# Kernel optimization log

Hardware: AMD Instinct MI355X
Metric: run time of the kernel (lower is better)

## Reference

```python
import jax, jax.numpy as jnp
import numpy as np

V = 8000; TZ = 128; TU = 256; B = 64; H = 1024; E = 512; DG = 64
GI = E + 2 * H + DG  # GRU input size = embed + z_ctx + u_ctx + degree


def _build_sparse_z(rng):
    # faithful vectorized version of get_sparse_selective_input (minus vocab SLOT branch)
    z_np = rng.integers(0, V + 10, size=(TZ, B))  # some ids >= V -> OOV copy path
    res = np.full((TZ, B, V + TZ), 1e-10, np.float32)
    w = z_np[:-1]                                   # [TZ-1, B]
    cond = (w == 2) | (w >= V)
    ti, bi = np.meshgrid(np.arange(TZ - 1), np.arange(B), indexing='ij')
    col = np.where(cond, V + ti, w)
    val = np.where(cond, np.float32(5.0), np.float32(1.0))
    res[ti + 1, bi, col] = val
    return jnp.asarray(res.transpose(1, 0, 2))      # [B, TZ, V+TZ]


def setup_inputs():
    key = jax.random.key(0)
    ks = jax.random.split(key, 16)
    s = 0.02
    iv = 1.0 / np.sqrt(H)
    return dict(
        z_enc_out=jax.random.normal(ks[0], (TZ, B, H), jnp.float32),
        u_enc_out=jax.random.normal(ks[1], (TU, B, H), jnp.float32),
        m_t_input=jax.random.randint(ks[2], (1, B), 0, V),
        degree_input=jax.random.normal(ks[3], (B, DG), jnp.float32),
        last_hidden=jax.random.normal(ks[4], (1, B, H), jnp.float32),
        sparse_z_input=_build_sparse_z(np.random.default_rng(0)),
        emb_W=jax.random.normal(ks[5], (V, E), jnp.float32) * s,
        attn_z_W=jax.random.normal(ks[6], (H, 2 * H), jnp.float32) * s,
        attn_z_b=jnp.zeros((H,), jnp.float32),
        attn_z_v=jax.random.normal(ks[7], (H,), jnp.float32) * iv,
        attn_u_W=jax.random.normal(ks[8], (H, 2 * H), jnp.float32) * s,
        attn_u_b=jnp.zeros((H,), jnp.float32),
        attn_u_v=jax.random.normal(ks[9], (H,), jnp.float32) * iv,
        gru_Wih=jax.random.normal(ks[10], (3 * H, GI), jnp.float32) * s,
        gru_Whh=jax.random.normal(ks[11], (3 * H, H), jnp.float32) * s,
        gru_bih=jnp.zeros((3 * H,), jnp.float32),
        gru_bhh=jnp.zeros((3 * H,), jnp.float32),
        proj_W=jax.random.normal(ks[12], (V, 3 * H), jnp.float32) * s,
        proj_b=jnp.zeros((V,), jnp.float32),
        copy2_W=jax.random.normal(ks[13], (H, H), jnp.float32) * s,
        copy2_b=jnp.zeros((H,), jnp.float32),
    )


def _attn(hidden, enc, W, b, v):
    # hidden [1,B,H], enc [T,B,H] -> context [1,B,H] (Bahdanau additive attention)
    enc_b = jnp.transpose(enc, (1, 0, 2))                       # [B,T,H]
    Hrep = jnp.broadcast_to(jnp.transpose(hidden, (1, 0, 2)), enc_b.shape)
    energy = jnp.tanh(jnp.concatenate([Hrep, enc_b], -1) @ W.T + b)  # [B,T,H]
    scores = jnp.einsum('bth,h->bt', energy, v)[:, None, :]    # [B,1,T]
    alpha = jax.nn.softmax(scores, axis=2)
    ctx = jnp.einsum('bit,bth->bih', alpha, enc_b)              # [B,1,H]
    return jnp.transpose(ctx, (1, 0, 2))                        # [1,B,H]


def _gru_step(x, h, Wih, Whh, bih, bhh):
    # single step, torch gate order (r, z, n)
    gi = x @ Wih.T + bih
    gh = h @ Whh.T + bhh
    ir, iz, inn = jnp.split(gi, 3, -1)
    hr, hz, hn = jnp.split(gh, 3, -1)
    r = jax.nn.sigmoid(ir + hr)
    z = jax.nn.sigmoid(iz + hz)
    n = jnp.tanh(inn + r * hn)
    return (1.0 - z) * n + z * h


def reference(z_enc_out, u_enc_out, m_t_input, degree_input, last_hidden,
              sparse_z_input, emb_W, attn_z_W, attn_z_b, attn_z_v,
              attn_u_W, attn_u_b, attn_u_v, gru_Wih, gru_Whh, gru_bih, gru_bhh,
              proj_W, proj_b, copy2_W, copy2_b):
    m_embed = emb_W[m_t_input]                                  # [1,B,E]
    z_ctx = _attn(last_hidden, z_enc_out, attn_z_W, attn_z_b, attn_z_v)  # [1,B,H]
    u_ctx = _attn(last_hidden, u_enc_out, attn_u_W, attn_u_b, attn_u_v)  # [1,B,H]
    gru_in = jnp.concatenate([m_embed, u_ctx, z_ctx, degree_input[None]], axis=2)
    gru_out = _gru_step(gru_in, last_hidden, gru_Wih, gru_Whh, gru_bih, gru_bhh)
    new_hidden = gru_out                                        # single-layer GRU, 1 step
    gen_score = (jnp.concatenate([z_ctx, u_ctx, gru_out], 2) @ proj_W.T + proj_b)[0]  # [B,V]
    # pointer copy scores over z encoder states
    z_cs = jnp.tanh(jnp.transpose(z_enc_out, (1, 0, 2)) @ copy2_W.T + copy2_b)  # [B,TZ,H]
    z_cs = jnp.einsum('bth,bh->bt', z_cs, gru_out[0])           # [B,TZ]
    m = jnp.max(z_cs, axis=1, keepdims=True)
    e = jnp.exp(z_cs - m)
    z_copy = jnp.log(jnp.einsum('bt,btv->bv', e, sparse_z_input)) + m  # [B,V+TZ]
    scores = jax.nn.softmax(jnp.concatenate([gen_score, z_copy], axis=1), axis=1)
    gen_s, zc = scores[:, :V], scores[:, V:]
    proba = jnp.concatenate([gen_s + zc[:, :V], zc[:, V:]], axis=1)  # [B, V+TZ]
    return (proba, new_hidden, gru_out)
```

## Files before the change

### kernel.cpp

```cpp
#include <hip/hip_runtime.h>
#include <cmath>

#define B64 64
#define H 1024
#define E 512
#define DG 64
#define GIN 2624
#define TZ 128
#define TU 256
#define V 8000
#define VT 8128
#define NC 16128

using bf16x8 = __attribute__((ext_vector_type(8))) short;
using f32x4  = __attribute__((ext_vector_type(4))) float;

__device__ inline unsigned pack2(float a, float b) {
    unsigned ua = __float_as_uint(a) + 0x8000u;
    unsigned ub = __float_as_uint(b) + 0x8000u;
    return __builtin_amdgcn_perm(ub, ua, 0x07060302u);
}
__device__ inline uint2 pack4(float4 v) {
    return make_uint2(pack2(v.x, v.y), pack2(v.z, v.w));
}

__device__ inline float fast_tanh(float x) {
    float e = __expf(2.f * x);
    return 1.f - 2.f / (e + 1.f);
}
__device__ inline float fast_sig(float x) {
    return 1.f / (1.f + __expf(-x));
}

__device__ inline void gl_lds16(const void* gptr, void* lptr) {
    __builtin_amdgcn_global_load_lds(
        (const __attribute__((address_space(1))) void*)gptr,
        (__attribute__((address_space(3))) void*)lptr, 16, 0, 0);
}

__global__ void k_cvt_all(const float* __restrict__ u_enc, const float* __restrict__ z_enc,
                          const float* __restrict__ azW, const float* __restrict__ auW,
                          const float* __restrict__ c2W,
                          unsigned short* __restrict__ ubf, unsigned short* __restrict__ zbf,
                          unsigned short* __restrict__ azWbf, unsigned short* __restrict__ auWbf,
                          unsigned short* __restrict__ c2Wbf,
                          const int* __restrict__ mt, const float* __restrict__ embW,
                          const float* __restrict__ degree, float* __restrict__ x)
{
    int n = blockIdx.x, tid = threadIdx.x;
    if (n >= 27648) {
        int b = n - 27648;
        int m = mt[b];
        for (int k = tid; k < E; k += 256) x[(size_t)b * GIN + k] = embW[(size_t)m * E + k];
        if (tid < DG) x[(size_t)b * GIN + E + 2 * H + tid] = degree[b * DG + tid];
        return;
    }
    int k4 = tid * 4;
    const float* src; unsigned short* dst; int ld, koff, r;
    if (n < 16384)      { src = u_enc; dst = ubf;   ld = 1024; koff = 0;    r = n; }
    else if (n < 24576) { src = z_enc; dst = zbf;   ld = 1024; koff = 0;    r = n - 16384; }
    else if (n < 25600) { src = azW;   dst = azWbf; ld = 2048; koff = 1024; r = n - 24576; }
    else if (n < 26624) { src = auW;   dst = auWbf; ld = 2048; koff = 1024; r = n - 25600; }
    else                { src = c2W;   dst = c2Wbf; ld = 1024; koff = 0;    r = n - 26624; }
    float4 v = *(const float4*)(src + (size_t)r * ld + koff + k4);
    *(uint2*)(dst + (size_t)r * 1024 + k4) = pack4(v);
}

__global__ __launch_bounds__(256) void ftd_all(
    const unsigned short* __restrict__ zbf_, const unsigned short* __restrict__ ubf_,
    const unsigned short* __restrict__ azWbf, const unsigned short* __restrict__ auWbf,
    const unsigned short* __restrict__ c2Wbf,
    const float* __restrict__ hbz, const float* __restrict__ hbu,
    const float* __restrict__ azv, const float* __restrict__ auv,
    const float* __restrict__ c2b,
    float* __restrict__ scores_z, float* __restrict__ scores_u,
    float* __restrict__ tz)
{
    __shared__ unsigned short As[128 * 32];
    __shared__ unsigned short Bs[128 * 32];
    const int tid  = threadIdx.x;
    const int wave = tid >> 6, lane = tid & 63;
    const int wm = wave >> 1, wn = wave & 1;
    const int q = lane >> 4, l16 = lane & 15;
    const int lrow = lane >> 2;
    const int lk   = (lane & 3) * 8;

    const int gid = blockIdx.x;
    const bool isU = gid >= 1024;
    int m0, n0;
    const unsigned short *A, *W;
    bool isTZ = false;
    const float* addv; const float* vvec; float* outs;
    if (isU) {
        int g = gid - 1024;
        m0 = (g & 127) * 128;
        n0 = (g >> 7) * 128;
        A = ubf_; W = auWbf;
        addv = hbu; vvec = auv; outs = scores_u;
    } else {
        m0 = (gid & 63) * 128;
        int by = gid >> 6;
        A = zbf_;
        if (by < 8) { n0 = by * 128; W = azWbf; addv = hbz; vvec = azv; outs = scores_z; }
        else        { n0 = (by - 8) * 128; W = c2Wbf; isTZ = true; addv = nullptr; vvec = nullptr; outs = nullptr; }
    }

    f32x4 acc[4][4];
#pragma unroll
    for (int i = 0; i < 4; ++i)
#pragma unroll
        for (int j = 0; j < 4; ++j) acc[i][j] = f32x4{0.f, 0.f, 0.f, 0.f};

    for (int kt = 0; kt < 32; ++kt) {
        const int k0 = kt * 32;
        __syncthreads();
#pragma unroll
        for (int j = 0; j < 2; ++j) {
            int r0 = (wave * 2 + j) * 16;
            gl_lds16(A + (size_t)(m0 + r0 + lrow) * 1024 + k0 + lk, &As[r0 * 32]);
            gl_lds16(W + (size_t)(n0 + r0 + lrow) * 1024 + k0 + lk, &Bs[r0 * 32]);
        }
        __syncthreads();
        bf16x8 af[4], bfr[4];
#pragma unroll
        for (int t = 0; t < 4; ++t) af[t]  = *(bf16x8*)&As[(wm * 64 + t * 16 + l16) * 32 + q * 8];
#pragma unroll
        for (int t = 0; t < 4; ++t) bfr[t] = *(bf16x8*)&Bs[(wn * 64 + t * 16 + l16) * 32 + q * 8];
#pragma unroll
        for (int tm = 0; tm < 4; ++tm)
#pragma unroll
            for (int tn = 0; tn < 4; ++tn)
                acc[tm][tn] = __builtin_amdgcn_mfma_f32_16x16x32_bf16(
                    af[tm], bfr[tn], acc[tm][tn], 0, 0, 0);
    }

    if (!isTZ) {
#pragma unroll
        for (int tm = 0; tm < 4; ++tm) {
#pragma unroll
            for (int r = 0; r < 4; ++r) {
                int R = m0 + wm * 64 + tm * 16 + q * 4 + r;
                int b = R & 63;
                float s = 0.f;
#pragma unroll
                for (int tn = 0; tn < 4; ++tn) {
                    int col = n0 + wn * 64 + tn * 16 + l16;
                    float e = acc[tm][tn][r] + addv[(size_t)b * 1024 + col];
                    s += fast_tanh(e) * vvec[col];
                }
                s += __shfl_xor(s, 1);
                s += __shfl_xor(s, 2);
                s += __shfl_xor(s, 4);
                s += __shfl_xor(s, 8);
                if (l16 == 0) atomicAdd(&outs[R], s);
            }
        }
    } else {
#pragma unroll
        for (int tm = 0; tm < 4; ++tm) {
#pragma unroll
            for (int r = 0; r < 4; ++r) {
                int R = m0 + wm * 64 + tm * 16 + q * 4 + r;
#pragma unroll
                for (int tn = 0; tn < 4; ++tn) {
                    int col = n0 + wn * 64 + tn * 16 + l16;
                    tz[(size_t)R * 1024 + col] = fast_tanh(acc[tm][tn][r] + c2b[col]);
                }
            }
        }
    }
}

__device__ __forceinline__ void gemm_core(
    short (*As)[40], short (*Bs)[40], int tid,
    const float* __restrict__ A, int lda,
    const float* __restrict__ W, int ldw, int koff,
    const float* __restrict__ bias,
    float* __restrict__ C, int N,
    int n0, int kb, int ke, bool addbias)
{
    const int wave = tid >> 6, lane = tid & 63;
    const int wm = wave >> 1, wn = wave & 1;
    const int q = lane >> 4, l16 = lane & 15;

    f32x4 acc[2][2];
#pragma unroll
    for (int i = 0; i < 2; ++i)
#pragma unroll
        for (int j = 0; j < 2; ++j) acc[i][j] = f32x4{0.f, 0.f, 0.f, 0.f};

    for (int ks = kb; ks < ke; ++ks) {
        const int k0 = ks * 32;
        __syncthreads();
#pragma unroll
        for (int i = 0; i < 2; ++i) {
            int slot = i * 256 + tid;
            int row  = slot >> 3;
            int kq   = (slot & 7) << 2;
            float4 a = *(const float4*)(A + (size_t)row * lda + k0 + kq);
            *(uint2*)&As[row][kq] = pack4(a);
            float4 w = *(const float4*)(W + (size_t)(n0 + row) * ldw + koff + k0 + kq);
            *(uint2*)&Bs[row][kq] = pack4(w);
        }
        __syncthreads();
        bf16x8 af[2], bfr[2];
#pragma unroll
        for (int t = 0; t < 2; ++t) af[t]  = *(bf16x8*)&As[wm * 32 + t * 16 + l16][q * 8];
#pragma unroll
        for (int t = 0; t < 2; ++t) bfr[t] = *(bf16x8*)&Bs[wn * 32 + t * 16 + l16][q * 8];
#pragma unroll
        for (int tm = 0; tm < 2; ++tm)
#pragma unroll
            for (int tn = 0; tn < 2; ++tn)
                acc[tm][tn] = __builtin_amdgcn_mfma_f32_16x16x32_bf16(
                    af[tm], bfr[tn], acc[tm][tn], 0, 0, 0);
    }

#pragma unroll
    for (int tm = 0; tm < 2; ++tm) {
#pragma unroll
        for (int r = 0; r < 4; ++r) {
            int b = wm * 32 + tm * 16 + q * 4 + r;
#pragma unroll
            for (int tn = 0; tn < 2; ++tn) {
                int n = n0 + wn * 32 + tn * 16 + l16;
                float v = acc[tm][tn][r];
                if (addbias) v += bias[n];
                atomicAdd(&C[(size_t)b * N + n], v);
            }
        }
    }
}

__global__ __launch_bounds__(256) void gemm_bt_mfma(
    const float* __restrict__ A, int lda,
    const float* __restrict__ W, int ldw, int koff,
    const float* __restrict__ bias,
    float* __restrict__ C, int N,
    int ks_total, int ks_chunk)
{
    __shared__ short As[64][40];
    __shared__ short Bs[64][40];
    int n0 = blockIdx.x * 64;
    int kb = blockIdx.y * ks_chunk;
    int ke = min(kb + ks_chunk, ks_total);
    gemm_core(As, Bs, threadIdx.x, A, lda, W, ldw, koff, bias, C, N,
              n0, kb, ke, blockIdx.y == 0);
}

__global__ __launch_bounds__(256) void gemm3(
    const float* __restrict__ h0,
    const float* __restrict__ azW, const float* __restrict__ azb, float* __restrict__ hbz,
    const float* __restrict__ auW, const float* __restrict__ aub, float* __restrict__ hbu,
    const float* __restrict__ Whh, const float* __restrict__ bhh, float* __restrict__ gh)
{
    __shared__ short As[64][40];
    __shared__ short Bs[64][40];
    int n = blockIdx.x;
    const float *W, *bias; float* C; int ldw, N, n0, kc;
    if (n < 128)      { W = azW; bias = azb; C = hbz; ldw = 2048; N = 1024; n0 = (n & 15) * 64;  kc = n >> 4; }
    else if (n < 256) { n -= 128; W = auW; bias = aub; C = hbu; ldw = 2048; N = 1024; n0 = (n & 15) * 64; kc = n >> 4; }
    else              { n -= 256; W = Whh; bias = bhh; C = gh;  ldw = 1024; N = 3072; n0 = (n % 48) * 64; kc = n / 48; }
    int kb = kc * 4, ke = kb + 4;
    gemm_core(As, Bs, threadIdx.x, h0, 1024, W, ldw, 0, bias, C, N, n0, kb, ke, kc == 0);
}

__global__ __launch_bounds__(256) void k_softmax_ctx_bf(
    const float* __restrict__ scores_z, const float* __restrict__ scores_u,
    const unsigned short* __restrict__ zbf_, const unsigned short* __restrict__ ubf_,
    float* __restrict__ x, float* __restrict__ y)
{
    __shared__ float red[256];
    __shared__ float al[256];
    int b = blockIdx.x, tid = threadIdx.x;
    int side = blockIdx.y >> 1, hc = blockIdx.y & 1;
    const float* scores = side ? scores_u : scores_z;
    const unsigned short* encbf = side ? ubf_ : zbf_;
    int T = side ? TU : TZ;
    int xoff = side ? 512 : 1536;
    int yoff = side ? 1024 : 0;

    float s = (tid < T) ? scores[tid * B64 + b] : -1e30f;
    red[tid] = s; __syncthreads();
    for (int off = 128; off > 0; off >>= 1) {
        if (tid < off) red[tid] = fmaxf(red[tid], red[tid + off]);
        __syncthreads();
    }
    float mx = red[0]; __syncthreads();
    float e = (tid < T) ? __expf(s - mx) : 0.f;
    red[tid] = e; __syncthreads();
    for (int off = 128; off > 0; off >>= 1) {
        if (tid < off) red[tid] += red[tid + off];
        __syncthreads();
    }
    float inv = 1.f / red[0];
    al[tid] = e * inv;
    __syncthreads();
    int h = hc * 512 + tid * 2;
    float a0 = 0.f, a1 = 0.f;
#pragma unroll 4
    for (int t = 0; t < T; ++t) {
        unsigned u = *(const unsigned*)(encbf + ((size_t)t * B64 + b) * 1024 + h);
        float w = al[t];
        a0 += w * __uint_as_float(u << 16);
        a1 += w * __uint_as_float(u & 0xffff0000u);
    }
    x[(size_t)b * GIN + xoff + h]     = a0;
    x[(size_t)b * GIN + xoff + h + 1] = a1;
    y[(size_t)b * 3072 + yoff + h]     = a0;
    y[(size_t)b * 3072 + yoff + h + 1] = a1;
}

__global__ void k_gate(const float* __restrict__ gi, const float* __restrict__ gh,
                       const float* __restrict__ h0, float* __restrict__ gru,
                       float* __restrict__ y, float* __restrict__ out_hid,
                       float* __restrict__ out_gru)
{
    int b = blockIdx.x, tid = threadIdx.x;
    for (int j = tid; j < H; j += 256) {
        float ir = gi[(size_t)b * 3072 + j];
        float iz = gi[(size_t)b * 3072 + H + j];
        float in_ = gi[(size_t)b * 3072 + 2 * H + j];
        float hr = gh[(size_t)b * 3072 + j];
        float hz = gh[(size_t)b * 3072 + H + j];
        float hn = gh[(size_t)b * 3072 + 2 * H + j];
        float r = fast_sig(ir + hr);
        float z = fast_sig(iz + hz);
        float n = fast_tanh(in_ + r * hn);
        float h = h0[(size_t)b * H + j];
        float o = (1.f - z) * n + z * h;
        gru[(size_t)b * H + j] = o;
        y[(size_t)b * 3072 + 2 * H + j] = o;
        out_hid[(size_t)b * H + j] = o;
        out_gru[(size_t)b * H + j] = o;
    }
}

__global__ __launch_bounds__(512) void k_zcs_dot(
    const float* __restrict__ tz, const float* __restrict__ gru,
    float* __restrict__ zraw)
{
    __shared__ float g[1024];
    int b = blockIdx.x, quarter = blockIdx.y, tid = threadIdx.x;
    int wave = tid >> 6, lane = tid & 63;
    for (int i = tid; i < 1024; i += 512) g[i] = gru[(size_t)b * 1024 + i];
    __syncthreads();
    float gr[16];
#pragma unroll
    for (int j = 0; j < 16; ++j) gr[j] = g[lane * 16 + j];
    int t0 = quarter * 32;
#pragma unroll
    for (int i = 0; i < 4; ++i) {
        int t = t0 + wave + i * 8;
        const float* row = tz + ((size_t)t * B64 + b) * 1024 + lane * 16;
        float s = 0.f;
#pragma unroll
        for (int c = 0; c < 4; ++c) {
            float4 v = *(const float4*)(row + c * 4);
            s += v.x * gr[c * 4 + 0] + v.y * gr[c * 4 + 1]
               + v.z * gr[c * 4 + 2] + v.w * gr[c * 4 + 3];
        }
#pragma unroll
        for (int off = 32; off > 0; off >>= 1) s += __shfl_xor(s, off);
        if (lane == 0) zraw[b * TZ + t] = s;
    }
}

__global__ __launch_bounds__(256) void k_sparse(
    const float* __restrict__ sz, const float* __restrict__ zraw,
    float* __restrict__ zcopy)
{
    __shared__ float es[TZ];
    __shared__ float mred[2];
    int c = blockIdx.x, b = blockIdx.y, tid = threadIdx.x;
    float sv = 0.f;
    if (tid < TZ) {
        sv = zraw[b * TZ + tid];
        float mm = sv;
#pragma unroll
        for (int off = 32; off > 0; off >>= 1) mm = fmaxf(mm, __shfl_xor(mm, off));
        if ((tid & 63) == 0) mred[tid >> 6] = mm;
    }
    __syncthreads();
    float m = fmaxf(mred[0], mred[1]);
    if (tid < TZ) es[tid] = __expf(sv - m);
    __syncthreads();
    if (tid >= 254) return;
    int v4 = c * 254 + tid;
    const f32x4* base = (const f32x4*)(sz + (size_t)b * TZ * VT);
    float4 acc = make_float4(0.f, 0.f, 0.f, 0.f);
#pragma unroll 16
    for (int t = 0; t < TZ; ++t) {
        f32x4 xv = __builtin_nontemporal_load(&base[(size_t)t * (VT / 4) + v4]);
        float e = es[t];
        acc.x += e * xv[0]; acc.y += e * xv[1]; acc.z += e * xv[2]; acc.w += e * xv[3];
    }
    int v = v4 * 4;
    zcopy[(size_t)b * VT + v + 0] = __logf(acc.x) + m;
    zcopy[(size_t)b * VT + v + 1] = __logf(acc.y) + m;
    zcopy[(size_t)b * VT + v + 2] = __logf(acc.z) + m;
    zcopy[(size_t)b * VT + v + 3] = __logf(acc.w) + m;
}

__global__ __launch_bounds__(1024) void k_final(
    const float* __restrict__ gen, const float* __restrict__ zcopy,
    float* __restrict__ proba)
{
    __shared__ float lg[NC];
    __shared__ float wred[16];
    int b = blockIdx.x, tid = threadIdx.x;
    int lane = tid & 63, wave = tid >> 6;
    for (int i = tid; i < V; i += 1024) lg[i] = gen[(size_t)b * V + i];
    for (int i = tid; i < VT; i += 1024) lg[V + i] = zcopy[(size_t)b * VT + i];
    __syncthreads();
    float mx = -1e30f;
    for (int i = tid; i < NC; i += 1024) mx = fmaxf(mx, lg[i]);
#pragma unroll
    for (int off = 32; off > 0; off >>= 1) mx = fmaxf(mx, __shfl_xor(mx, off));
    if (lane == 0) wred[wave] = mx;
    __syncthreads();
    mx = wred[0];
#pragma unroll
    for (int w = 1; w < 16; ++w) mx = fmaxf(mx, wred[w]);
    __syncthreads();
    float sm = 0.f;
    for (int i = tid; i < NC; i += 1024) sm += __expf(lg[i] - mx);
#pragma unroll
    for (int off = 32; off > 0; off >>= 1) sm += __shfl_xor(sm, off);
    if (lane == 0) wred[wave] = sm;
    __syncthreads();
    float Z = 0.f;
#pragma unroll
    for (int w = 0; w < 16; ++w) Z += wred[w];
    float invZ = 1.f / Z;
    for (int v = tid; v < VT; v += 1024) {
        float p = __expf(lg[V + v] - mx) * invZ;
        if (v < V) p += __expf(lg[v] - mx) * invZ;
        proba[(size_t)b * VT + v] = p;
    }
}

extern "C" void kernel_launch(void* const* d_in, const int* in_sizes, int n_in,
                              void* d_out, int out_size, void* d_ws, size_t ws_size,
                              hipStream_t stream)
{
    const float* z_enc  = (const float*)d_in[0];
    const float* u_enc  = (const float*)d_in[1];
    const int*   mt     = (const int*)d_in[2];
    const float* degree = (const float*)d_in[3];
    const float* h0     = (const float*)d_in[4];
    const float* sz     = (const float*)d_in[5];
    const float* embW   = (const float*)d_in[6];
    const float* azW    = (const float*)d_in[7];
    const float* azb    = (const float*)d_in[8];
    const float* azv    = (const float*)d_in[9];
    const float* auW    = (const float*)d_in[10];
    const float* aub    = (const float*)d_in[11];
    const float* auv    = (const float*)d_in[12];
    const float* Wih    = (const float*)d_in[13];
    const float* Whh    = (const float*)d_in[14];
    const float* bih    = (const float*)d_in[15];
    const float* bhh    = (const float*)d_in[16];
    const float* pW     = (const float*)d_in[17];
    const float* pb     = (const float*)d_in[18];
    const float* c2W    = (const float*)d_in[19];
    const float* c2b    = (const float*)d_in[20];

    float* ws       = (float*)d_ws;
    float* scores_z = ws;
    float* scores_u = ws + 8192;
    float* hbz      = ws + 32768;
    float* hbu      = ws + 98304;
    float* gi       = ws + 163840;
    float* gh       = ws + 360448;
    float* gen      = ws + 557056;
    float* x        = ws + 1069056;
    float* y        = ws + 1236992;
    float* gru      = ws + 1433600;
    float* zcopy    = ws + 1507392;
    float* tz       = ws + 2027584;
    unsigned short* ubf   = (unsigned short*)(ws + 2027584 + 8388608);
    unsigned short* zbf   = ubf + (size_t)16384 * 1024;
    unsigned short* azWbf = zbf + (size_t)8192 * 1024;
    unsigned short* auWbf = azWbf + (size_t)1024 * 1024;
    unsigned short* c2Wbf = auWbf + (size_t)1024 * 1024;
    float* zraw = ws + 24571968;

    float* out_proba = (float*)d_out;
    float* out_hid   = out_proba + (size_t)B64 * VT;
    float* out_gru   = out_hid + (size_t)B64 * H;

    hipMemsetAsync(ws, 0, 1069056 * sizeof(float), stream);

    k_cvt_all<<<27712, 256, 0, stream>>>(u_enc, z_enc, azW, auW, c2W,
                                         ubf, zbf, azWbf, auWbf, c2Wbf,
                                         mt, embW, degree, x);

    gemm3<<<640, 256, 0, stream>>>(h0, azW, azb, hbz, auW, aub, hbu, Whh, bhh, gh);

    ftd_all<<<2048, 256, 0, stream>>>(zbf, ubf, azWbf, auWbf, c2Wbf,
                                      hbz, hbu, azv, auv, c2b,
                                      scores_z, scores_u, tz);

    k_softmax_ctx_bf<<<dim3(64, 4), 256, 0, stream>>>(scores_z, scores_u, zbf, ubf, x, y);

    gemm_bt_mfma<<<dim3(48, 8), 256, 0, stream>>>(x, GIN, Wih, GIN, 0, bih, gi, 3072, 82, 11);
    k_gate<<<64, 256, 0, stream>>>(gi, gh, h0, gru, y, out_hid, out_gru);

    k_zcs_dot<<<dim3(64, 4), 512, 0, stream>>>(tz, gru, zraw);

    gemm_bt_mfma<<<dim3(125, 8), 256, 0, stream>>>(y, 3072, pW, 3072, 0, pb, gen, 8000, 96, 12);

    k_sparse<<<dim3(8, 64), 256, 0, stream>>>(sz, zraw, zcopy);

    k_final<<<64, 1024, 0, stream>>>(gen, zcopy, out_proba);
}
```

Before: 770.3 us.

## Merge independent kernels to cut launch count and overlap phases

Folds the three small h0 GEMMs into the bf16 conversion kernel, fuses the GRU gate with the z-copy dot product (each quarter block recomputes the gate into shared memory), and runs the projection GEMM and the sparse copy reduction as one heterogeneous grid. The aim is fewer kernel launches and less idle tail time, since independent work can now share the GPU. The cost is redundant gate recomputation across four blocks per batch row and mixed-workload grids whose blocks vary in shared-memory needs and duration.

```diff
diff --git a/kernel.cpp b/kernel.cpp
--- a/kernel.cpp
+++ b/kernel.cpp
@@ -38,16 +38,94 @@
         (__attribute__((address_space(3))) void*)lptr, 16, 0, 0);
 }
 
-__global__ void k_cvt_all(const float* __restrict__ u_enc, const float* __restrict__ z_enc,
-                          const float* __restrict__ azW, const float* __restrict__ auW,
-                          const float* __restrict__ c2W,
-                          unsigned short* __restrict__ ubf, unsigned short* __restrict__ zbf,
-                          unsigned short* __restrict__ azWbf, unsigned short* __restrict__ auWbf,
-                          unsigned short* __restrict__ c2Wbf,
-                          const int* __restrict__ mt, const float* __restrict__ embW,
-                          const float* __restrict__ degree, float* __restrict__ x)
-{
+__device__ __forceinline__ void gemm_core(
+    short (*As)[40], short (*Bs)[40], int tid,
+    const float* __restrict__ A, int lda,
+    const float* __restrict__ W, int ldw, int koff,
+    const float* __restrict__ bias,
+    float* __restrict__ C, int N,
+    int n0, int kb, int ke, bool addbias)
+{
+    const int wave = tid >> 6, lane = tid & 63;
+    const int wm = wave >> 1, wn = wave & 1;
+    const int q = lane >> 4, l16 = lane & 15;
+
+    f32x4 acc[2][2];
+#pragma unroll
+    for (int i = 0; i < 2; ++i)
+#pragma unroll
+        for (int j = 0; j < 2; ++j) acc[i][j] = f32x4{0.f, 0.f, 0.f, 0.f};
+
+    for (int ks = kb; ks < ke; ++ks) {
+        const int k0 = ks * 32;
+        __syncthreads();
+#pragma unroll
+        for (int i = 0; i < 2; ++i) {
+            int slot = i * 256 + tid;
+            int row  = slot >> 3;
+            int kq   = (slot & 7) << 2;
+            float4 a = *(const float4*)(A + (size_t)row * lda + k0 + kq);
+            *(uint2*)&As[row][kq] = pack4(a);
+            float4 w = *(const float4*)(W + (size_t)(n0 + row) * ldw + koff + k0 + kq);
+            *(uint2*)&Bs[row][kq] = pack4(w);
+        }
+        __syncthreads();
+        bf16x8 af[2], bfr[2];
+#pragma unroll
+        for (int t = 0; t < 2; ++t) af[t]  = *(bf16x8*)&As[wm * 32 + t * 16 + l16][q * 8];
+#pragma unroll
+        for (int t = 0; t < 2; ++t) bfr[t] = *(bf16x8*)&Bs[wn * 32 + t * 16 + l16][q * 8];
+#pragma unroll
+        for (int tm = 0; tm < 2; ++tm)
+#pragma unroll
+            for (int tn = 0; tn < 2; ++tn)
+                acc[tm][tn] = __builtin_amdgcn_mfma_f32_16x16x32_bf16(
+                    af[tm], bfr[tn], acc[tm][tn], 0, 0, 0);
+    }
+
+#pragma unroll
+    for (int tm = 0; tm < 2; ++tm) {
+#pragma unroll
+        for (int r = 0; r < 4; ++r) {
+            int b = wm * 32 + tm * 16 + q * 4 + r;
+#pragma unroll
+            for (int tn = 0; tn < 2; ++tn) {
+                int n = n0 + wn * 32 + tn * 16 + l16;
+                float v = acc[tm][tn][r];
+                if (addbias) v += bias[n];
+                atomicAdd(&C[(size_t)b * N + n], v);
+            }
+        }
+    }
+}
+
+__global__ __launch_bounds__(256) void k_prep(
+    const float* __restrict__ u_enc, const float* __restrict__ z_enc,
+    const float* __restrict__ azW, const float* __restrict__ auW,
+    const float* __restrict__ c2W,
+    unsigned short* __restrict__ ubf, unsigned short* __restrict__ zbf,
+    unsigned short* __restrict__ azWbf, unsigned short* __restrict__ auWbf,
+    unsigned short* __restrict__ c2Wbf,
+    const int* __restrict__ mt, const float* __restrict__ embW,
+    const float* __restrict__ degree, float* __restrict__ x,
+    const float* __restrict__ h0,
+    const float* __restrict__ azb, float* __restrict__ hbz,
+    const float* __restrict__ aub, float* __restrict__ hbu,
+    const float* __restrict__ Whh, const float* __restrict__ bhh,
+    float* __restrict__ gh)
+{
+    __shared__ short As[64][40];
+    __shared__ short Bs[64][40];
     int n = blockIdx.x, tid = threadIdx.x;
+    if (n < 640) {
+        const float *W, *bias; float* C; int ldw, N, n0, kc;
+        if (n < 128)      { W = azW; bias = azb; C = hbz; ldw = 2048; N = 1024; n0 = (n & 15) * 64;  kc = n >> 4; }
+        else if (n < 256) { int m = n - 128; W = auW; bias = aub; C = hbu; ldw = 2048; N = 1024; n0 = (m & 15) * 64; kc = m >> 4; }
+        else              { int m = n - 256; W = Whh; bias = bhh; C = gh;  ldw = 1024; N = 3072; n0 = (m % 48) * 64; kc = m / 48; }
+        gemm_core(As, Bs, tid, h0, 1024, W, ldw, 0, bias, C, N, n0, kc * 4, kc * 4 + 4, kc == 0);
+        return;
+    }
+    n -= 640;
     if (n >= 27648) {
         int b = n - 27648;
         int m = mt[b];
@@ -171,67 +249,6 @@
     }
 }
 
-__device__ __forceinline__ void gemm_core(
-    short (*As)[40], short (*Bs)[40], int tid,
-    const float* __restrict__ A, int lda,
-    const float* __restrict__ W, int ldw, int koff,
-    const float* __restrict__ bias,
-    float* __restrict__ C, int N,
-    int n0, int kb, int ke, bool addbias)
-{
-    const int wave = tid >> 6, lane = tid & 63;
-    const int wm = wave >> 1, wn = wave & 1;
-    const int q = lane >> 4, l16 = lane & 15;
-
-    f32x4 acc[2][2];
-#pragma unroll
-    for (int i = 0; i < 2; ++i)
-#pragma unroll
-        for (int j = 0; j < 2; ++j) acc[i][j] = f32x4{0.f, 0.f, 0.f, 0.f};
-
-    for (int ks = kb; ks < ke; ++ks) {
-        const int k0 = ks * 32;
-        __syncthreads();
-#pragma unroll
-        for (int i = 0; i < 2; ++i) {
-            int slot = i * 256 + tid;
-            int row  = slot >> 3;
-            int kq   = (slot & 7) << 2;
-            float4 a = *(const float4*)(A + (size_t)row * lda + k0 + kq);
-            *(uint2*)&As[row][kq] = pack4(a);
-            float4 w = *(const float4*)(W + (size_t)(n0 + row) * ldw + koff + k0 + kq);
-            *(uint2*)&Bs[row][kq] = pack4(w);
-        }
-        __syncthreads();
-        bf16x8 af[2], bfr[2];
-#pragma unroll
-        for (int t = 0; t < 2; ++t) af[t]  = *(bf16x8*)&As[wm * 32 + t * 16 + l16][q * 8];
-#pragma unroll
-        for (int t = 0; t < 2; ++t) bfr[t] = *(bf16x8*)&Bs[wn * 32 + t * 16 + l16][q * 8];
-#pragma unroll
-        for (int tm = 0; tm < 2; ++tm)
-#pragma unroll
-            for (int tn = 0; tn < 2; ++tn)
-                acc[tm][tn] = __builtin_amdgcn_mfma_f32_16x16x32_bf16(
-                    af[tm], bfr[tn], acc[tm][tn], 0, 0, 0);
-    }
-
-#pragma unroll
-    for (int tm = 0; tm < 2; ++tm) {
-#pragma unroll
-        for (int r = 0; r < 4; ++r) {
-            int b = wm * 32 + tm * 16 + q * 4 + r;
-#pragma unroll
-            for (int tn = 0; tn < 2; ++tn) {
-                int n = n0 + wn * 32 + tn * 16 + l16;
-                float v = acc[tm][tn][r];
-                if (addbias) v += bias[n];
-                atomicAdd(&C[(size_t)b * N + n], v);
-            }
-        }
-    }
-}
-
 __global__ __launch_bounds__(256) void gemm_bt_mfma(
     const float* __restrict__ A, int lda,
     const float* __restrict__ W, int ldw, int koff,
@@ -246,23 +263,6 @@
     int ke = min(kb + ks_chunk, ks_total);
     gemm_core(As, Bs, threadIdx.x, A, lda, W, ldw, koff, bias, C, N,
               n0, kb, ke, blockIdx.y == 0);
-}
-
-__global__ __launch_bounds__(256) void gemm3(
-    const float* __restrict__ h0,
-    const float* __restrict__ azW, const float* __restrict__ azb, float* __restrict__ hbz,
-    const float* __restrict__ auW, const float* __restrict__ aub, float* __restrict__ hbu,
-    const float* __restrict__ Whh, const float* __restrict__ bhh, float* __restrict__ gh)
-{
-    __shared__ short As[64][40];
-    __shared__ short Bs[64][40];
-    int n = blockIdx.x;
-    const float *W, *bias; float* C; int ldw, N, n0, kc;
-    if (n < 128)      { W = azW; bias = azb; C = hbz; ldw = 2048; N = 1024; n0 = (n & 15) * 64;  kc = n >> 4; }
-    else if (n < 256) { n -= 128; W = auW; bias = aub; C = hbu; ldw = 2048; N = 1024; n0 = (n & 15) * 64; kc = n >> 4; }
-    else              { n -= 256; W = Whh; bias = bhh; C = gh;  ldw = 1024; N = 3072; n0 = (n % 48) * 64; kc = n / 48; }
-    int kb = kc * 4, ke = kb + 4;
-    gemm_core(As, Bs, threadIdx.x, h0, 1024, W, ldw, 0, bias, C, N, n0, kb, ke, kc == 0);
 }
 
 __global__ __launch_bounds__(256) void k_softmax_ctx_bf(
@@ -311,13 +311,17 @@
     y[(size_t)b * 3072 + yoff + h + 1] = a1;
 }
 
-__global__ void k_gate(const float* __restrict__ gi, const float* __restrict__ gh,
-                       const float* __restrict__ h0, float* __restrict__ gru,
-                       float* __restrict__ y, float* __restrict__ out_hid,
-                       float* __restrict__ out_gru)
-{
-    int b = blockIdx.x, tid = threadIdx.x;
-    for (int j = tid; j < H; j += 256) {
+__global__ __launch_bounds__(512) void k_zcs_gate(
+    const float* __restrict__ gi, const float* __restrict__ gh,
+    const float* __restrict__ h0, const float* __restrict__ tz,
+    float* __restrict__ zraw,
+    float* __restrict__ y, float* __restrict__ out_hid,
+    float* __restrict__ out_gru)
+{
+    __shared__ float g[1024];
+    int b = blockIdx.x, quarter = blockIdx.y, tid = threadIdx.x;
+    int wave = tid >> 6, lane = tid & 63;
+    for (int j = tid; j < H; j += 512) {
         float ir = gi[(size_t)b * 3072 + j];
         float iz = gi[(size_t)b * 3072 + H + j];
         float in_ = gi[(size_t)b * 3072 + 2 * H + j];
@@ -326,24 +330,16 @@
         float hn = gh[(size_t)b * 3072 + 2 * H + j];
         float r = fast_sig(ir + hr);
         float z = fast_sig(iz + hz);
-        float n = fast_tanh(in_ + r * hn);
+        float nn = fast_tanh(in_ + r * hn);
         float h = h0[(size_t)b * H + j];
-        float o = (1.f - z) * n + z * h;
-        gru[(size_t)b * H + j] = o;
-        y[(size_t)b * 3072 + 2 * H + j] = o;
-        out_hid[(size_t)b * H + j] = o;
-        out_gru[(size_t)b * H + j] = o;
-    }
-}
-
-__global__ __launch_bounds__(512) void k_zcs_dot(
-    const float* __restrict__ tz, const float* __restrict__ gru,
-    float* __restrict__ zraw)
-{
-    __shared__ float g[1024];
-    int b = blockIdx.x, quarter = blockIdx.y, tid = threadIdx.x;
-    int wave = tid >> 6, lane = tid & 63;
-    for (int i = tid; i < 1024; i += 512) g[i] = gru[(size_t)b * 1024 + i];
+        float o = (1.f - z) * nn + z * h;
+        g[j] = o;
+        if (quarter == 0) {
+            y[(size_t)b * 3072 + 2 * H + j] = o;
+            out_hid[(size_t)b * H + j] = o;
+            out_gru[(size_t)b * H + j] = o;
+        }
+    }
     __syncthreads();
     float gr[16];
 #pragma unroll
@@ -366,13 +362,26 @@
     }
 }
 
-__global__ __launch_bounds__(256) void k_sparse(
+__global__ __launch_bounds__(256) void k_gen_sparse(
+    const float* __restrict__ y, const float* __restrict__ pW,
+    const float* __restrict__ pb, float* __restrict__ gen,
     const float* __restrict__ sz, const float* __restrict__ zraw,
     float* __restrict__ zcopy)
 {
+    __shared__ short As[64][40];
+    __shared__ short Bs[64][40];
     __shared__ float es[TZ];
     __shared__ float mred[2];
-    int c = blockIdx.x, b = blockIdx.y, tid = threadIdx.x;
+    int n = blockIdx.x, tid = threadIdx.x;
+    if (n >= 512) {
+        int gblk = n - 512;
+        int n0 = (gblk % 125) * 64;
+        int kc = gblk / 125;
+        gemm_core(As, Bs, tid, y, 3072, pW, 3072, 0, pb, gen, 8000,
+                  n0, kc * 12, kc * 12 + 12, kc == 0);
+        return;
+    }
+    int c = n & 7, b = n >> 3;
     float sv = 0.f;
     if (tid < TZ) {
         sv = zraw[b * TZ + tid];
@@ -476,7 +485,6 @@
     float* gen      = ws + 557056;
     float* x        = ws + 1069056;
     float* y        = ws + 1236992;
-    float* gru      = ws + 1433600;
     float* zcopy    = ws + 1507392;
     float* tz       = ws + 2027584;
     unsigned short* ubf   = (unsigned short*)(ws + 2027584 + 8388608);
@@ -492,11 +500,10 @@
 
     hipMemsetAsync(ws, 0, 1069056 * sizeof(float), stream);
 
-    k_cvt_all<<<27712, 256, 0, stream>>>(u_enc, z_enc, azW, auW, c2W,
-                                         ubf, zbf, azWbf, auWbf, c2Wbf,
-                                         mt, embW, degree, x);
-
-    gemm3<<<640, 256, 0, stream>>>(h0, azW, azb, hbz, auW, aub, hbu, Whh, bhh, gh);
+    k_prep<<<28352, 256, 0, stream>>>(u_enc, z_enc, azW, auW, c2W,
+                                      ubf, zbf, azWbf, auWbf, c2Wbf,
+                                      mt, embW, degree, x,
+                                      h0, azb, hbz, aub, hbu, Whh, bhh, gh);
 
     ftd_all<<<2048, 256, 0, stream>>>(zbf, ubf, azWbf, auWbf, c2Wbf,
                                       hbz, hbu, azv, auv, c2b,
@@ -505,13 +512,10 @@
     k_softmax_ctx_bf<<<dim3(64, 4), 256, 0, stream>>>(scores_z, scores_u, zbf, ubf, x, y);
 
     gemm_bt_mfma<<<dim3(48, 8), 256, 0, stream>>>(x, GIN, Wih, GIN, 0, bih, gi, 3072, 82, 11);
-    k_gate<<<64, 256, 0, stream>>>(gi, gh, h0, gru, y, out_hid, out_gru);
-
-    k_zcs_dot<<<dim3(64, 4), 512, 0, stream>>>(tz, gru, zraw);
-
-    gemm_bt_mfma<<<dim3(125, 8), 256, 0, stream>>>(y, 3072, pW, 3072, 0, pb, gen, 8000, 96, 12);
-
-    k_sparse<<<dim3(8, 64), 256, 0, stream>>>(sz, zraw, zcopy);
+
+    k_zcs_gate<<<dim3(64, 4), 512, 0, stream>>>(gi, gh, h0, tz, zraw, y, out_hid, out_gru);
+
+    k_gen_sparse<<<1512, 256, 0, stream>>>(y, pW, pb, gen, sz, zraw, zcopy);
 
     k_final<<<64, 1024, 0, stream>>>(gen, zcopy, out_proba);
 }
```

Measured after the change: 744.4 us. 1.03x faster.
